# Performance work log

Measured on AMD Instinct MI355X. Metric: run time of the kernel, lower is better.

Reference implementation:

```python
import jax, jax.numpy as jnp
from jax import lax
import numpy as np

DN = ('NCHW', 'OIHW', 'NCHW')
K = 3          # deformable kernel size
DG = 4         # deform groups
EXP = 4        # InvBottle expansion


def conv_offset(x, w1, w2, b2):
    """InvBottle with diff=True: depthwise-expanded 3x3 conv, diff correction, 1x1 conv."""
    B, C, H, W = x.shape
    _x = lax.conv_general_dilated(x, w1, (1, 1), ((1, 1), (1, 1)),
                                  dimension_numbers=DN, feature_group_count=C)  # [B,4C,H,W]
    # diff_conv: subtract grouped 1x1 conv with the kernel-summed weight
    wsum = w1.sum((2, 3)).reshape(1, EXP * C, 1, 1)          # [1,4C,1,1]
    xd = _x - jnp.repeat(x, EXP, axis=1) * wsum              # group g uses input channel g
    t = lax.conv_general_dilated(xd, w2, (1, 1), ((0, 0), (0, 0)), dimension_numbers=DN)
    return t + b2.reshape(1, -1, 1, 1)                       # [B,72,H,W]


def deform_depthwise(x, off, w, pad=1):
    """Depthwise DeformConv2d (groups=C, deform_groups=DG), stride=1, dilation=1."""
    B, C, H, W = x.shape
    Cg = C // DG
    off = off.reshape(B, DG, K * K, 2, H, W)                 # (dy, dx) interleaved per tap
    dy, dx = off[:, :, :, 0], off[:, :, :, 1]                # [B,DG,9,H,W]
    ky = (jnp.arange(K * K) // K).reshape(1, 1, K * K, 1, 1).astype(x.dtype)
    kx = (jnp.arange(K * K) % K).reshape(1, 1, K * K, 1, 1).astype(x.dtype)
    py = jnp.arange(H, dtype=x.dtype).reshape(1, 1, 1, H, 1) - pad + ky + dy
    px = jnp.arange(W, dtype=x.dtype).reshape(1, 1, 1, 1, W) - pad + kx + dx

    y0 = jnp.floor(py)
    x0 = jnp.floor(px)
    wy = py - y0
    wx = px - x0

    xg = x.reshape(B, DG, Cg, H * W)

    def gather(yy, xx):
        valid = ((yy >= 0) & (yy < H) & (xx >= 0) & (xx < W)).astype(x.dtype)
        yc = jnp.clip(yy, 0, H - 1).astype(jnp.int32)
        xc = jnp.clip(xx, 0, W - 1).astype(jnp.int32)
        idx = (yc * W + xc).reshape(B, DG, 1, K * K * H * W)
        v = jnp.take_along_axis(xg, jnp.broadcast_to(idx, (B, DG, Cg, K * K * H * W)), axis=3)
        return v.reshape(B, DG, Cg, K * K, H, W) * valid[:, :, None]

    val = (gather(y0, x0) * ((1 - wy) * (1 - wx))[:, :, None]
           + gather(y0, x0 + 1) * ((1 - wy) * wx)[:, :, None]
           + gather(y0 + 1, x0) * (wy * (1 - wx))[:, :, None]
           + gather(y0 + 1, x0 + 1) * (wy * wx)[:, :, None])   # [B,DG,Cg,9,H,W]

    val = val.reshape(B, C, K * K, H, W)
    return jnp.einsum('bckhw,ck->bchw', val, w.reshape(C, K * K))


def setup_inputs() -> dict:
    key = jax.random.key(0)
    ks = jax.random.split(key, 6)
    B, C, H, W = 2, 64, 192, 192
    x1 = jax.random.normal(ks[0], (B, C, H, W), jnp.float32)
    w_off1 = jax.random.normal(ks[1], (EXP * C, 1, K, K), jnp.float32) * 0.1
    w_off2 = jax.random.normal(ks[2], (DG * 2 * K * K, EXP * C, 1, 1), jnp.float32) * 0.1
    b_off2 = jax.random.normal(ks[3], (DG * 2 * K * K,), jnp.float32) * 0.1
    w_def = jax.random.normal(ks[4], (C, 1, K, K), jnp.float32) * 0.1
    w_out = jax.random.normal(ks[5], (C, C, 1, 1), jnp.float32) * 0.1
    return {'x1': x1, 'w_off1': w_off1, 'w_off2': w_off2, 'b_off2': b_off2,
            'w_def': w_def, 'w_out': w_out}


def reference(x1, w_off1, w_off2, b_off2, w_def, w_out):
    x2 = x1
    C = x1.shape[1]
    t = conv_offset(x1, w_off1, w_off2, b_off2)              # [B,72,H,W]
    y = deform_depthwise(x1, t, w_def)                       # DeformConv2d, groups=C
    # diff_conv against the deform conv's kernel-summed depthwise weight
    y = y - x2 * w_def.sum((1, 2, 3)).reshape(1, C, 1, 1)
    m = jnp.einsum('bchw,oc->bohw', y, w_out.reshape(w_out.shape[0], C))  # 1x1, no bias
    return (x1, m)
```

## Files before the change

### kernel.cpp

```cpp
#include <hip/hip_runtime.h>

#define BN   2
#define CN   64
#define HN   192
#define WN   192
#define HWN  36864
#define OCN  256
#define JCN  72
#define SN   32

#define DROWS 8
#define XH    17
#define XW    42
#define XRT   4
#define XCL   4

typedef __attribute__((ext_vector_type(8))) short bf16x8;
typedef __attribute__((ext_vector_type(4))) float f32x4;

__device__ __forceinline__ unsigned short f2bf(float f) {
    union { float f; unsigned u; } v; v.f = f;
    unsigned r = v.u + 0x7fffu + ((v.u >> 16) & 1u);
    return (unsigned short)(r >> 16);
}

__global__ __launch_bounds__(256) void k_prep(const float* __restrict__ w2,
                                              const float* __restrict__ w_out,
                                              const float* __restrict__ w1,
                                              unsigned short* __restrict__ w2mf,
                                              unsigned short* __restrict__ w_outmf,
                                              float* __restrict__ w1p) {
    int idx = blockIdx.x * 256 + threadIdx.x;
    if (idx < 20480) {
        int j  = idx & 7;
        int l  = (idx >> 3) & 63;
        int ts = idx >> 9;
        int tm = ts >> 3, s = ts & 7;
        int jrow = tm * 16 + (l & 15);
        int k    = s * 32 + (l >> 4) * 8 + j;
        float v = (jrow < JCN) ? w2[jrow * OCN + k] : 0.f;
        w2mf[idx] = f2bf(v);
    } else if (idx < 24576) {
        int r  = idx - 20480;
        int j  = r & 7;
        int l  = (r >> 3) & 63;
        int ts = r >> 9;
        int tm = ts >> 1, s = ts & 1;
        int m  = tm * 16 + (l & 15);
        int k  = s * 32 + (l >> 4) * 8 + j;
        w_outmf[r] = f2bf(w_out[m * CN + k]);
    } else if (idx < 26624) {
        int r = idx - 24576;
        int o = r >> 3, kk = r & 7;
        int k = kk < 4 ? kk : kk + 1;
        w1p[r] = w1[o * 9 + k];
    }
}

__global__ __launch_bounds__(256, 4) void k_offsets(const float* __restrict__ x,
                                                    const float* __restrict__ w1p,
                                                    const unsigned short* __restrict__ w2mf,
                                                    const float* __restrict__ b2,
                                                    float* __restrict__ t_out,
                                                    float* __restrict__ x_copy) {
    const int tid  = threadIdx.x;
    const int wv   = tid >> 6;
    const int lane = tid & 63;
    const int q    = lane >> 4;
    const int n    = lane & 15;
    const int n0   = blockIdx.x * 64 + wv * 16;
    const int y    = blockIdx.y;
    const int b    = blockIdx.z;
    const int xcol = n0 + n;
    const float* xb = x + (size_t)b * CN * HWN;

    auto load_chunk = [&](int s, float (*ld)[9]) {
        #pragma unroll
        for (int cc = 0; cc < 2; ++cc) {
            int c = 8 * s + 2 * q + cc;
            const float* xp = xb + (size_t)c * HWN;
            #pragma unroll
            for (int k = 0; k < 9; ++k) {
                int ky = k / 3, kx = k - 3 * ky;
                int yy = y - 1 + ky, xx = xcol - 1 + kx;
                float v = 0.f;
                if ((unsigned)yy < (unsigned)HN && (unsigned)xx < (unsigned)WN)
                    v = xp[yy * WN + xx];
                ld[cc][k] = v;
            }
        }
    };

    f32x4 acc[5];
    #pragma unroll
    for (int t = 0; t < 5; ++t) acc[t] = (f32x4){0.f, 0.f, 0.f, 0.f};

    const bf16x8* ap = (const bf16x8*)w2mf + lane;

    float lbuf[2][2][9];
    load_chunk(0, lbuf[0]);
    #pragma unroll
    for (int s = 0; s < 8; ++s) {
        if (s < 7) load_chunk(s + 1, lbuf[(s + 1) & 1]);
        float (*ld)[9] = lbuf[s & 1];

        float dd[2][8];
        #pragma unroll
        for (int cc = 0; cc < 2; ++cc) {
            int c = 8 * s + 2 * q + cc;
            float ctr = ld[cc][4];
            x_copy[((size_t)b * CN + c) * HWN + y * WN + xcol] = ctr;
            #pragma unroll
            for (int kk = 0; kk < 8; ++kk) {
                int k = kk < 4 ? kk : kk + 1;
                dd[cc][kk] = ld[cc][k] - ctr;
            }
        }

        bf16x8 bfr;
        const float4* wp = (const float4*)(w1p + (size_t)(s * 32 + q * 8) * 8);
        #pragma unroll
        for (int j = 0; j < 8; ++j) {
            float4 wa = wp[2 * j];
            float4 wb = wp[2 * j + 1];
            const float* d = dd[j >> 2];
            float a = wa.x * d[0] + wa.y * d[1] + wa.z * d[2] + wa.w * d[3]
                    + wb.x * d[4] + wb.y * d[5] + wb.z * d[6] + wb.w * d[7];
            bfr[j] = (short)f2bf(a);
        }

        #pragma unroll
        for (int tm = 0; tm < 5; ++tm) {
            bf16x8 af = ap[(tm * 8 + s) * 64];
            acc[tm] = __builtin_amdgcn_mfma_f32_16x16x32_bf16(af, bfr, acc[tm], 0, 0, 0);
        }
    }

    float* tb = t_out + (size_t)b * JCN * HWN + y * WN + n0 + n;
    #pragma unroll
    for (int tm = 0; tm < 5; ++tm) {
        #pragma unroll
        for (int r = 0; r < 4; ++r) {
            int j = tm * 16 + q * 4 + r;
            if (j < JCN)
                tb[(size_t)j * HWN] = acc[tm][r] + b2[j];
        }
    }
}

__device__ __forceinline__ float dsample(const float* __restrict__ p, int yi, int xi) {
    if ((unsigned)yi < (unsigned)HN && (unsigned)xi < (unsigned)WN)
        return p[yi * WN + xi];
    return 0.f;
}

__global__ __launch_bounds__(256, 4) void k_deform(const float* __restrict__ x,
                                                   const float* __restrict__ t_in,
                                                   const float* __restrict__ wdef,
                                                   float* __restrict__ y_out) {
    __shared__ float xs[8 * XH * XW];
    __shared__ float wks[9 * 8];
    __shared__ float wsums[8];
    const int x0   = blockIdx.x * SN;
    const int yr0  = blockIdx.y * DROWS;
    const int zz   = blockIdx.z;
    const int b    = zz >> 3;
    const int chunk = zz & 7;
    const int g    = chunk >> 1;
    const int tid  = threadIdx.x;
    const int r    = tid >> 5;
    const int px   = tid & 31;
    const int row_lo = yr0 - XRT;
    const int col_lo = x0 - XCL;
    const float* xb = x + (size_t)b * CN * HWN;

    float dyr[9], dxr[9];
    {
        const float* tbp = t_in + ((size_t)b * JCN + g * 18) * HWN
                         + (yr0 + r) * WN + x0 + px;
        #pragma unroll
        for (int k = 0; k < 9; ++k) {
            dyr[k] = tbp[(size_t)(2 * k) * HWN];
            dxr[k] = tbp[(size_t)(2 * k + 1) * HWN];
        }
    }

    for (int idx = tid; idx < 8 * XH * XW; idx += 256) {
        int cc  = idx / (XH * XW);
        int rem = idx - cc * (XH * XW);
        int rr  = rem / XW;
        int col = rem - rr * XW;
        int yy  = row_lo + rr;
        int xx  = col_lo + col;
        float v = 0.f;
        if ((unsigned)yy < (unsigned)HN && (unsigned)xx < (unsigned)WN)
            v = xb[(size_t)(chunk * 8 + cc) * HWN + yy * WN + xx];
        xs[idx] = v;
    }
    if (tid < 72) {
        int k = tid >> 3, cc = tid & 7;
        wks[tid] = wdef[(chunk * 8 + cc) * 9 + k];
    } else if (tid < 80) {
        int cc = tid - 72;
        float s = 0.f;
        #pragma unroll
        for (int k = 0; k < 9; ++k) s += wdef[(chunk * 8 + cc) * 9 + k];
        wsums[cc] = s;
    }
    __syncthreads();

    float acc[8];
    #pragma unroll
    for (int c = 0; c < 8; ++c)
        acc[c] = -xs[c * (XH * XW) + (XRT + r) * XW + XCL + px] * wsums[c];

    const float ry_basef = (float)(yr0 + r - 1);
    const float rx_basef = (float)(x0 + px - 1);

    #pragma unroll
    for (int k = 0; k < 9; ++k) {
        const int ky = k / 3, kx = k - 3 * ky;
        float py  = ry_basef + (float)ky + dyr[k];
        float pxf = rx_basef + (float)kx + dxr[k];
        float y0f = floorf(py), x0f = floorf(pxf);
        float wy = py - y0f, wx = pxf - x0f;
        int yi = (int)y0f, xi = (int)x0f;
        int ry = yi - row_lo, rx = xi - col_lo;
        float omwy = 1.f - wy, omwx = 1.f - wx;
        float w00 = omwy * omwx;
        float w01 = omwy * wx;
        float w10 = wy * omwx;
        float w11 = wy * wx;
        float4 wka = *(const float4*)&wks[k * 8];
        float4 wkb = *(const float4*)&wks[k * 8 + 4];
        float wkv[8] = {wka.x, wka.y, wka.z, wka.w, wkb.x, wkb.y, wkb.z, wkb.w};
        if ((unsigned)ry < (XH - 1) && (unsigned)rx < (XW - 1)) {
            const float* p0 = xs + ry * XW + rx;
            #pragma unroll
            for (int c = 0; c < 8; ++c) {
                const float* p = p0 + c * (XH * XW);
                float bil = p[0] * w00 + p[1] * w01 + p[XW] * w10 + p[XW + 1] * w11;
                acc[c] += wkv[c] * bil;
            }
        } else {
            #pragma unroll
            for (int c = 0; c < 8; ++c) {
                const float* xp = xb + (size_t)(chunk * 8 + c) * HWN;
                float v00 = dsample(xp, yi,     xi);
                float v01 = dsample(xp, yi,     xi + 1);
                float v10 = dsample(xp, yi + 1, xi);
                float v11 = dsample(xp, yi + 1, xi + 1);
                float bil = v00 * w00 + v01 * w01 + v10 * w10 + v11 * w11;
                acc[c] += wkv[c] * bil;
            }
        }
    }

    float* yo = y_out + ((size_t)b * CN + chunk * 8) * HWN + (yr0 + r) * WN + x0 + px;
    #pragma unroll
    for (int c = 0; c < 8; ++c)
        yo[(size_t)c * HWN] = acc[c];
}

__global__ __launch_bounds__(256, 8) void k_final(const float* __restrict__ y_in,
                                                  const unsigned short* __restrict__ womf,
                                                  float* __restrict__ m_out) {
    const int tid  = threadIdx.x;
    const int wv   = tid >> 6;
    const int lane = tid & 63;
    const int q    = lane >> 4;
    const int n    = lane & 15;
    const int n0   = blockIdx.x * 64 + wv * 16;
    const int yr   = blockIdx.y;
    const int b    = blockIdx.z;

    const float* yb = y_in + (size_t)b * CN * HWN + yr * WN + n0 + n;

    float yv[2][8];
    #pragma unroll
    for (int s = 0; s < 2; ++s)
        #pragma unroll
        for (int j = 0; j < 8; ++j)
            yv[s][j] = yb[(size_t)(s * 32 + q * 8 + j) * HWN];

    bf16x8 bfr[2];
    #pragma unroll
    for (int s = 0; s < 2; ++s)
        #pragma unroll
        for (int j = 0; j < 8; ++j)
            bfr[s][j] = (short)f2bf(yv[s][j]);

    const bf16x8* ap = (const bf16x8*)womf + lane;
    f32x4 acc[4];
    #pragma unroll
    for (int tm = 0; tm < 4; ++tm) acc[tm] = (f32x4){0.f, 0.f, 0.f, 0.f};
    #pragma unroll
    for (int tm = 0; tm < 4; ++tm) {
        #pragma unroll
        for (int s = 0; s < 2; ++s) {
            bf16x8 af = ap[(tm * 2 + s) * 64];
            acc[tm] = __builtin_amdgcn_mfma_f32_16x16x32_bf16(af, bfr[s], acc[tm], 0, 0, 0);
        }
    }

    float* mb = m_out + (size_t)b * CN * HWN + yr * WN + n0 + n;
    #pragma unroll
    for (int tm = 0; tm < 4; ++tm) {
        #pragma unroll
        for (int r = 0; r < 4; ++r)
            mb[(size_t)(tm * 16 + q * 4 + r) * HWN] = acc[tm][r];
    }
}

extern "C" void kernel_launch(void* const* d_in, const int* in_sizes, int n_in,
                              void* d_out, int out_size, void* d_ws, size_t ws_size,
                              hipStream_t stream) {
    const float* x1    = (const float*)d_in[0];
    const float* w_off1 = (const float*)d_in[1];
    const float* w_off2 = (const float*)d_in[2];
    const float* b_off2 = (const float*)d_in[3];
    const float* w_def = (const float*)d_in[4];
    const float* w_out = (const float*)d_in[5];

    float* out = (float*)d_out;
    const size_t n_x = (size_t)BN * CN * HWN;
    float* out_x1 = out;
    float* out_m  = out + n_x;

    char* ws0 = (char*)d_ws;
    unsigned short* w2mf   = (unsigned short*)ws0;
    unsigned short* w_outmf = (unsigned short*)(ws0 + 40960);
    float* w1p    = (float*)(ws0 + 49152);
    float* t_ws   = (float*)(ws0 + 57344);
    float* y_ws   = t_ws + (size_t)BN * JCN * HWN;

    dim3 blk(256);

    k_prep<<<dim3(104), blk, 0, stream>>>(w_off2, w_out, w_off1, w2mf, w_outmf, w1p);
    k_offsets<<<dim3(WN / 64, HN, BN), blk, 0, stream>>>(x1, w1p, w2mf, b_off2,
                                                         t_ws, out_x1);
    k_deform<<<dim3(WN / SN, HN / DROWS, BN * 8), blk, 0, stream>>>(x1, t_ws, w_def, y_ws);
    k_final<<<dim3(WN / 64, HN, BN), blk, 0, stream>>>(y_ws, w_outmf, out_m);
}
```

Before: 182.1 us.

## Store deform output as bf16 and vectorize offset-kernel neighborhood loads

The deform kernel now writes its intermediate result as bf16 instead of fp32, and the final 1x1 MFMA kernel reads bf16 directly without converting. This halves the intermediate's write and read traffic, and the rounding is the same one k_final already applied before its bf16 MFMA. Separately, the offset kernel loads each 3x3 row with one 2-float vector load plus one scalar load, using edge-clamped bases, instead of nine guarded scalar loads. The vector load at lbase may be unaligned to 8 bytes, which the aligned(4) type allows.

```diff
diff --git a/kernel.cpp b/kernel.cpp
--- a/kernel.cpp
+++ b/kernel.cpp
@@ -17,6 +17,7 @@
 
 typedef __attribute__((ext_vector_type(8))) short bf16x8;
 typedef __attribute__((ext_vector_type(4))) float f32x4;
+typedef float f2u __attribute__((ext_vector_type(2), aligned(4)));
 
 __device__ __forceinline__ unsigned short f2bf(float f) {
     union { float f; unsigned u; } v; v.f = f;
@@ -74,19 +75,31 @@
     const int xcol = n0 + n;
     const float* xb = x + (size_t)b * CN * HWN;
 
+    const bool edgeL = (xcol == 0);
+    const bool edgeR = (xcol == WN - 1);
+    const int  lbase = edgeL ? 0 : xcol - 1;
+    const int  rbase = edgeR ? WN - 1 : xcol + 1;
+
     auto load_chunk = [&](int s, float (*ld)[9]) {
         #pragma unroll
         for (int cc = 0; cc < 2; ++cc) {
             int c = 8 * s + 2 * q + cc;
             const float* xp = xb + (size_t)c * HWN;
             #pragma unroll
-            for (int k = 0; k < 9; ++k) {
-                int ky = k / 3, kx = k - 3 * ky;
-                int yy = y - 1 + ky, xx = xcol - 1 + kx;
-                float v = 0.f;
-                if ((unsigned)yy < (unsigned)HN && (unsigned)xx < (unsigned)WN)
-                    v = xp[yy * WN + xx];
-                ld[cc][k] = v;
+            for (int r = 0; r < 3; ++r) {
+                int yy = y - 1 + r;
+                float vl = 0.f, vm = 0.f, vr = 0.f;
+                if ((unsigned)yy < (unsigned)HN) {
+                    const float* rp = xp + yy * WN;
+                    f2u  p2 = *(const f2u*)(rp + lbase);
+                    float rv = rp[rbase];
+                    vm = edgeL ? p2.x : p2.y;
+                    vl = edgeL ? 0.f : p2.x;
+                    vr = edgeR ? 0.f : rv;
+                }
+                ld[cc][r * 3 + 0] = vl;
+                ld[cc][r * 3 + 1] = vm;
+                ld[cc][r * 3 + 2] = vr;
             }
         }
     };
@@ -157,7 +170,7 @@
 __global__ __launch_bounds__(256, 4) void k_deform(const float* __restrict__ x,
                                                    const float* __restrict__ t_in,
                                                    const float* __restrict__ wdef,
-                                                   float* __restrict__ y_out) {
+                                                   unsigned short* __restrict__ y_out) {
     __shared__ float xs[8 * XH * XW];
     __shared__ float wks[9 * 8];
     __shared__ float wsums[8];
@@ -256,13 +269,13 @@
         }
     }
 
-    float* yo = y_out + ((size_t)b * CN + chunk * 8) * HWN + (yr0 + r) * WN + x0 + px;
+    unsigned short* yo = y_out + ((size_t)b * CN + chunk * 8) * HWN + (yr0 + r) * WN + x0 + px;
     #pragma unroll
     for (int c = 0; c < 8; ++c)
-        yo[(size_t)c * HWN] = acc[c];
-}
-
-__global__ __launch_bounds__(256, 8) void k_final(const float* __restrict__ y_in,
+        yo[(size_t)c * HWN] = f2bf(acc[c]);
+}
+
+__global__ __launch_bounds__(256, 8) void k_final(const unsigned short* __restrict__ y_in,
                                                   const unsigned short* __restrict__ womf,
                                                   float* __restrict__ m_out) {
     const int tid  = threadIdx.x;
@@ -274,21 +287,14 @@
     const int yr   = blockIdx.y;
     const int b    = blockIdx.z;
 
-    const float* yb = y_in + (size_t)b * CN * HWN + yr * WN + n0 + n;
-
-    float yv[2][8];
+    const unsigned short* yb = y_in + (size_t)b * CN * HWN + yr * WN + n0 + n;
+
+    bf16x8 bfr[2];
     #pragma unroll
     for (int s = 0; s < 2; ++s)
         #pragma unroll
         for (int j = 0; j < 8; ++j)
-            yv[s][j] = yb[(size_t)(s * 32 + q * 8 + j) * HWN];
-
-    bf16x8 bfr[2];
-    #pragma unroll
-    for (int s = 0; s < 2; ++s)
-        #pragma unroll
-        for (int j = 0; j < 8; ++j)
-            bfr[s][j] = (short)f2bf(yv[s][j]);
+            bfr[s][j] = (short)yb[(size_t)(s * 32 + q * 8 + j) * HWN];
 
     const bf16x8* ap = (const bf16x8*)womf + lane;
     f32x4 acc[4];
@@ -332,7 +338,7 @@
     unsigned short* w_outmf = (unsigned short*)(ws0 + 40960);
     float* w1p    = (float*)(ws0 + 49152);
     float* t_ws   = (float*)(ws0 + 57344);
-    float* y_ws   = t_ws + (size_t)BN * JCN * HWN;
+    unsigned short* y_ws = (unsigned short*)(ws0 + 57344 + (size_t)BN * JCN * HWN * 4);
 
     dim3 blk(256);
 
```

New measurement: 200.6 us. 1.1x slower.
